# Kernel tuning notes

Hardware: AMD Instinct MI355X
Metric: run time of the kernel (lower is better)

The kernel has to match this reference:

```python
import jax, jax.numpy as jnp
import numpy as np

B = 4
C = 128           # input channels
H = W = 512       # image size
P = 16            # patch size
GH = GW = 32      # token grid (H//P, W//P)
N = GH * GW       # num patches = 1024
PATCH_DIM = C * P * P  # 32768
DIM = 512         # embed dim
MLP = 256         # ffn hidden
DH = 64           # dim per head
HEADS = (2, 4, 8) # per-layer head counts
NUM_REL = (2 * GH - 1) * (2 * GW - 1)  # 3969


def _rel_index():
    # faithful to the torch buffer construction (meshgrid default 'ij')
    coords = np.stack(np.meshgrid(np.arange(GH), np.arange(GW), indexing='ij')).reshape(2, -1)
    rc = (coords[:, :, None] - coords[:, None, :]).transpose(1, 2, 0)  # [N,N,2]
    rc[..., 0] += GH - 1
    rc[..., 1] += GW - 1
    rc[..., 0] *= 2 * GH - 1
    return jnp.asarray(rc.sum(-1))  # [N,N] int

REL_IDX = _rel_index()


def _ln(x, s, b):
    m = x.mean(-1, keepdims=True)
    v = x.var(-1, keepdims=True)
    return (x - m) / jnp.sqrt(v + 1e-5) * s + b


def setup_inputs() -> dict:
    key = jax.random.key(0)
    ks = iter(jax.random.split(key, 40))
    def rn(shape, scale=0.02):
        return jax.random.normal(next(ks), shape, jnp.float32) * scale
    inp = {"img": jax.random.normal(next(ks), (B, C, H, W), jnp.float32)}
    inp["patch_w"] = rn((PATCH_DIM, DIM))
    inp["patch_b"] = jnp.zeros((DIM,), jnp.float32)
    inp["pos_emb"] = rn((1, N, DIM), 1.0)
    inp["ln1_s"] = jnp.ones((3, DIM), jnp.float32)
    inp["ln1_b"] = jnp.zeros((3, DIM), jnp.float32)
    inp["ln2_s"] = jnp.ones((3, DIM), jnp.float32)
    inp["ln2_b"] = jnp.zeros((3, DIM), jnp.float32)
    for l, h in enumerate(HEADS):
        inner = DH * h
        inp[f"qkv_w{l}"] = rn((DIM, 3 * inner))
        inp[f"out_w{l}"] = rn((inner, DIM))
        inp[f"out_b{l}"] = jnp.zeros((DIM,), jnp.float32)
        inp[f"bias{l}"] = rn((NUM_REL, h))
    inp["ff_w1"] = rn((3, DIM, MLP))
    inp["ff_b1"] = jnp.zeros((3, MLP), jnp.float32)
    inp["ff_w2"] = rn((3, MLP, DIM))
    inp["ff_b2"] = jnp.zeros((3, DIM), jnp.float32)
    return inp


def reference(img, patch_w, patch_b, pos_emb, ln1_s, ln1_b, ln2_s, ln2_b,
              qkv_w0, qkv_w1, qkv_w2, out_w0, out_w1, out_w2,
              out_b0, out_b1, out_b2, bias0, bias1, bias2,
              ff_w1, ff_b1, ff_w2, ff_b2):
    b = img.shape[0]
    # Rearrange 'b c (h p1) (w p2) -> b (h w) (p1 p2 c)'
    x = img.reshape(b, C, GH, P, GW, P).transpose(0, 2, 4, 3, 5, 1).reshape(b, N, PATCH_DIM)
    x = x @ patch_w + patch_b + pos_emb

    qkv_ws = (qkv_w0, qkv_w1, qkv_w2)
    out_ws = (out_w0, out_w1, out_w2)
    out_bs = (out_b0, out_b1, out_b2)
    tables = (bias0, bias1, bias2)

    for l, h in enumerate(HEADS):
        # attention with relative position bias
        xn = _ln(x, ln1_s[l], ln1_b[l])
        qkv = xn @ qkv_ws[l]                                  # [b, N, 3*h*DH]
        q, k, v = jnp.split(qkv, 3, axis=-1)
        q = q.reshape(b, N, h, DH).transpose(0, 2, 1, 3)      # bhnd
        k = k.reshape(b, N, h, DH).transpose(0, 2, 1, 3)
        v = v.reshape(b, N, h, DH).transpose(0, 2, 1, 3)
        dots = jnp.einsum('bhnd,bhmd->bhnm', q, k) * (DH ** -0.5)
        rel = tables[l][REL_IDX].transpose(2, 0, 1)           # [h, N, N]
        attn = jax.nn.softmax(dots + rel[None], axis=-1)
        o = jnp.einsum('bhnm,bhmd->bhnd', attn, v)
        o = o.transpose(0, 2, 1, 3).reshape(b, N, h * DH)
        x = o @ out_ws[l] + out_bs[l] + x
        # feed-forward
        xn = _ln(x, ln2_s[l], ln2_b[l])
        hmid = jax.nn.gelu(xn @ ff_w1[l] + ff_b1[l], approximate=False)
        x = hmid @ ff_w2[l] + ff_b2[l] + x

    return x.transpose(0, 2, 1).reshape(b, DIM, GH, GW)
```

## Files before the change

### kernel.cpp

```cpp
#include <hip/hip_runtime.h>

typedef unsigned short u16;
typedef __bf16 bf16x8 __attribute__((ext_vector_type(8)));
typedef float f32x4 __attribute__((ext_vector_type(4)));

#define AS1 __attribute__((address_space(1)))
#define AS3 __attribute__((address_space(3)))
#define MFMA(a,b,c) __builtin_amdgcn_mfma_f32_16x16x32_bf16(a,b,c,0,0,0)

__device__ __forceinline__ u16 f2bf(float f) {
    union { float f; unsigned u; } x; x.f = f;
    unsigned r = x.u + 0x7fffu + ((x.u >> 16) & 1u);
    return (u16)(r >> 16);
}

__global__ void k_patch_wT(const float* __restrict__ w, u16* __restrict__ o)
{
    __shared__ u16 T[256*33];
    int c = blockIdx.x, n0 = blockIdx.y*32;
    int t = threadIdx.x;
    int rr = t >> 5, cc = t & 31;
    #pragma unroll
    for (int i = 0; i < 32; ++i) {
        int r = i*8 + rr;
        int k = (r >> 4)*2048 + (r & 15)*128 + c;
        T[r*33 + cc] = f2bf(w[(size_t)k*512 + n0 + cc]);
    }
    __syncthreads();
    #pragma unroll
    for (int i = 0; i < 4; ++i) {
        int j  = i*8 + (t >> 5);
        int ch = t & 31;
        union { u16 u[8]; uint4 v; } pk;
        #pragma unroll
        for (int q = 0; q < 8; ++q) pk.u[q] = T[(ch*8+q)*33 + j];
        *(uint4*)(o + (size_t)(n0 + j)*32768 + c*256 + ch*8) = pk.v;
    }
}

struct TXJob { const float* in; u16* out; int K, N, tiles; };
struct TXArgs { TXJob j[12]; };

__global__ void k_wT_all(TXArgs a)
{
    __shared__ float T[32*33];
    int bid = blockIdx.x;
    int ji = 0;
    while (bid >= a.j[ji].tiles) { bid -= a.j[ji].tiles; ++ji; }
    const float* __restrict__ in = a.j[ji].in;
    u16* __restrict__ o = a.j[ji].out;
    const int K = a.j[ji].K, N = a.j[ji].N;
    const int tn = N >> 5;
    const int kt = (bid / tn) * 32, nt = (bid % tn) * 32;
    int t = threadIdx.x, r = t >> 5, c = t & 31;
    #pragma unroll
    for (int i = 0; i < 4; ++i)
        T[(r + i*8)*33 + c] = in[(size_t)(kt + r + i*8)*N + nt + c];
    __syncthreads();
    #pragma unroll
    for (int i = 0; i < 4; ++i)
        o[(size_t)(nt + r + i*8)*K + kt + c] = f2bf(T[c*33 + r + i*8]);
}

__global__ __launch_bounds__(1024) void k_patch_gemm(
    const float* __restrict__ img, const u16* __restrict__ Bt, float* __restrict__ part)
{
    __shared__ alignas(16) u16 As[2*128*64];
    __shared__ alignas(16) u16 Bs[2*512*64];
    const int t = threadIdx.x;
    const int bid = blockIdx.x;
    const int z = bid & 7;
    const int tile = bid >> 3;
    const int b = tile >> 3, gh0 = (tile & 7)*4;
    const int m0 = tile*128;
    const int wave = t >> 6, lane = t & 63;
    const int r16 = lane & 15, g = lane >> 4;
    const int wm = (wave >> 3)*64, wn = (wave & 7)*64;

    const int arow = t >> 6;
    const int ghl = arow >> 2, p1l = arow & 3;
    const int aw = (t & 63)*8;
    const int tok = ghl*32 + (aw >> 4);
    unsigned abyte = (unsigned)(tok*128 + p1l*32 + (aw & 15)*2);
    abyte ^= (unsigned)((tok & 7) << 4);
    const float* imgb = img + (size_t)b*128*262144
                      + (size_t)((gh0 + ghl)*16 + p1l)*512 + aw;
    const int brow = t >> 3;
    const int bchunk = (t & 7) ^ (brow & 7);
    const u16* Bb = Bt + (size_t)brow*32768 + (size_t)z*4096 + bchunk*8;
    u16* Bsd = Bs + t*8;

    f32x4 acc[4][4];
    const f32x4 zz = {0.f,0.f,0.f,0.f};
    #pragma unroll
    for (int im = 0; im < 4; ++im)
        #pragma unroll
        for (int in_ = 0; in_ < 4; ++in_) acc[im][in_] = zz;

#define STAGE(KC, BUF) do {                                                          \
    const int c_ = z*16 + ((KC) >> 2);                                               \
    const float* src_ = imgb + (size_t)c_*262144 + ((KC) & 3)*2048;                  \
    float4 a0_ = *(const float4*)src_;                                               \
    float4 a1_ = *(const float4*)(src_ + 4);                                         \
    _Pragma("unroll")                                                                \
    for (int i_ = 0; i_ < 4; ++i_)                                                   \
        __builtin_amdgcn_global_load_lds((AS1 void*)(Bb + (size_t)i_*128*32768 + (KC)*64), \
                                         (AS3 void*)(Bsd + (BUF)*32768 + i_*8192), 16, 0, 0); \
    union { u16 u[8]; uint4 v; } pk_;                                                \
    pk_.u[0]=f2bf(a0_.x); pk_.u[1]=f2bf(a0_.y); pk_.u[2]=f2bf(a0_.z); pk_.u[3]=f2bf(a0_.w); \
    pk_.u[4]=f2bf(a1_.x); pk_.u[5]=f2bf(a1_.y); pk_.u[6]=f2bf(a1_.z); pk_.u[7]=f2bf(a1_.w); \
    *(uint4*)((char*)As + (BUF)*16384 + abyte) = pk_.v;                              \
} while(0)

    STAGE(0, 0);
    __syncthreads();
    int cur = 0;
    for (int kc = 0; kc < 64; ++kc) {
        if (kc < 63) STAGE(kc + 1, cur ^ 1);
        const char* Asb = (const char*)As + cur*16384;
        const char* Bsb = (const char*)Bs + cur*65536;
        #pragma unroll
        for (int kk = 0; kk < 64; kk += 32) {
            bf16x8 af[4], bfr[4];
            #pragma unroll
            for (int im = 0; im < 4; ++im) {
                unsigned off = ((unsigned)((wm + im*16 + r16)*128 + kk*2 + g*16))
                             ^ (unsigned)((r16 & 7) << 4);
                af[im] = *(const bf16x8*)(Asb + off);
            }
            #pragma unroll
            for (int in_ = 0; in_ < 4; ++in_) {
                unsigned off = ((unsigned)((wn + in_*16 + r16)*128 + kk*2 + g*16))
                             ^ (unsigned)((r16 & 7) << 4);
                bfr[in_] = *(const bf16x8*)(Bsb + off);
            }
            #pragma unroll
            for (int im = 0; im < 4; ++im)
                #pragma unroll
                for (int in_ = 0; in_ < 4; ++in_)
                    acc[im][in_] = MFMA(af[im], bfr[in_], acc[im][in_]);
        }
        __syncthreads();
        cur ^= 1;
    }
#undef STAGE
    float* pz = part + (size_t)z*4096*512;
    #pragma unroll
    for (int im = 0; im < 4; ++im) {
        int row = m0 + wm + im*16 + g*4;
        #pragma unroll
        for (int in_ = 0; in_ < 4; ++in_) {
            int col = wn + in_*16 + r16;
            #pragma unroll
            for (int r = 0; r < 4; ++r)
                pz[(size_t)(row + r)*512 + col] = acc[im][in_][r];
        }
    }
}

__global__ void k_reduce_ln(const float* __restrict__ part,
                            const float* __restrict__ pb, const float* __restrict__ pe,
                            const float* __restrict__ sc, const float* __restrict__ bi,
                            float* __restrict__ x, u16* __restrict__ xn)
{
    int row = blockIdx.x, lane = threadIdx.x;
    int d = lane*8;
    size_t rbase = (size_t)row*512 + d;
    float4 a0 = *(const float4*)(pb + d);
    float4 a1 = *(const float4*)(pb + d + 4);
    size_t pebase = (size_t)(row & 1023)*512 + d;
    float4 p0 = *(const float4*)(pe + pebase);
    float4 p1 = *(const float4*)(pe + pebase + 4);
    float vv[8] = {a0.x+p0.x, a0.y+p0.y, a0.z+p0.z, a0.w+p0.w,
                   a1.x+p1.x, a1.y+p1.y, a1.z+p1.z, a1.w+p1.w};
    #pragma unroll
    for (int z = 0; z < 8; ++z) {
        const float* pr = part + (size_t)z*4096*512 + rbase;
        float4 q0 = *(const float4*)pr;
        float4 q1 = *(const float4*)(pr + 4);
        vv[0] += q0.x; vv[1] += q0.y; vv[2] += q0.z; vv[3] += q0.w;
        vv[4] += q1.x; vv[5] += q1.y; vv[6] += q1.z; vv[7] += q1.w;
    }
    float4 w0 = make_float4(vv[0], vv[1], vv[2], vv[3]);
    float4 w1 = make_float4(vv[4], vv[5], vv[6], vv[7]);
    *(float4*)(x + rbase) = w0;
    *(float4*)(x + rbase + 4) = w1;
    float sum = 0.f, sq = 0.f;
    #pragma unroll
    for (int i = 0; i < 8; ++i) { sum += vv[i]; sq += vv[i]*vv[i]; }
    #pragma unroll
    for (int m = 1; m < 64; m <<= 1) { sum += __shfl_xor(sum, m, 64); sq += __shfl_xor(sq, m, 64); }
    float mean = sum * (1.f/512.f);
    float var  = sq  * (1.f/512.f) - mean*mean;
    float rstd = rsqrtf(var + 1e-5f);
    union { u16 u[8]; uint4 v; } pk;
    #pragma unroll
    for (int i = 0; i < 8; ++i) pk.u[i] = f2bf((vv[i]-mean)*rstd*sc[d+i] + bi[d+i]);
    *(uint4*)(xn + rbase) = pk.v;
}

__global__ void k_ln(const float* __restrict__ x, const float* __restrict__ sc,
                     const float* __restrict__ bi, u16* __restrict__ o)
{
    int row = blockIdx.x, lane = threadIdx.x;
    const float* xr = x + (size_t)row*512 + lane*8;
    float4 v0 = *(const float4*)xr;
    float4 v1 = *(const float4*)(xr + 4);
    float vv[8] = {v0.x,v0.y,v0.z,v0.w,v1.x,v1.y,v1.z,v1.w};
    float sum = 0.f, sq = 0.f;
    #pragma unroll
    for (int i = 0; i < 8; ++i) { sum += vv[i]; sq += vv[i]*vv[i]; }
    #pragma unroll
    for (int m = 1; m < 64; m <<= 1) { sum += __shfl_xor(sum, m, 64); sq += __shfl_xor(sq, m, 64); }
    float mean = sum * (1.f/512.f);
    float var  = sq  * (1.f/512.f) - mean*mean;
    float rstd = rsqrtf(var + 1e-5f);
    int d = lane*8;
    union { u16 u[8]; uint4 v; } pk;
    #pragma unroll
    for (int i = 0; i < 8; ++i) pk.u[i] = f2bf((vv[i]-mean)*rstd*sc[d+i] + bi[d+i]);
    *(uint4*)(o + (size_t)row*512 + d) = pk.v;
}

template<int EPI, int KB>
__global__ __launch_bounds__(256) void k_gemm(
    const u16* __restrict__ A, int lda,
    const u16* __restrict__ Bt, int ldb,
    float* __restrict__ Cf, u16* __restrict__ Cb, int ldc,
    const float* __restrict__ bias)
{
    __shared__ alignas(16) u16 As[128*64];
    __shared__ alignas(16) u16 Bs[128*64];
    const int t = threadIdx.x;
    const int m0 = blockIdx.x*128, n0 = blockIdx.y*128;
    const int wave = t >> 6, lane = t & 63;
    const int wm = (wave >> 1)*64, wn = (wave & 1)*64;
    const int r16 = lane & 15, g = lane >> 4;
    const u16* Ab = A + (size_t)(m0 + (t>>3))*lda + (t&7)*8;
    const u16* Bb = Bt + (size_t)(n0 + (t>>3))*ldb + (t&7)*8;
    u16* Asd = As + t*8;
    u16* Bsd = Bs + t*8;
    f32x4 acc[4][4];
    const f32x4 z4 = {0.f,0.f,0.f,0.f};
    #pragma unroll
    for (int im = 0; im < 4; ++im)
        #pragma unroll
        for (int in_ = 0; in_ < 4; ++in_) acc[im][in_] = z4;

    #pragma unroll
    for (int k = 0; k < KB; k += 64) {
        #pragma unroll
        for (int i = 0; i < 4; ++i) {
            __builtin_amdgcn_global_load_lds((AS1 void*)(Ab + (size_t)i*32*lda + k), (AS3 void*)(Asd + i*2048), 16, 0, 0);
            __builtin_amdgcn_global_load_lds((AS1 void*)(Bb + (size_t)i*32*ldb + k), (AS3 void*)(Bsd + i*2048), 16, 0, 0);
        }
        __syncthreads();
        #pragma unroll
        for (int kk = 0; kk < 64; kk += 32) {
            bf16x8 af[4], bfr[4];
            #pragma unroll
            for (int im = 0; im < 4; ++im)
                af[im] = *(const bf16x8*)(As + (wm + im*16 + r16)*64 + kk + g*8);
            #pragma unroll
            for (int in_ = 0; in_ < 4; ++in_)
                bfr[in_] = *(const bf16x8*)(Bs + (wn + in_*16 + r16)*64 + kk + g*8);
            #pragma unroll
            for (int im = 0; im < 4; ++im)
                #pragma unroll
                for (int in_ = 0; in_ < 4; ++in_)
                    acc[im][in_] = MFMA(af[im], bfr[in_], acc[im][in_]);
        }
        __syncthreads();
    }
    #pragma unroll
    for (int im = 0; im < 4; ++im) {
        int row = m0 + wm + im*16 + g*4;
        #pragma unroll
        for (int in_ = 0; in_ < 4; ++in_) {
            int col = n0 + wn + in_*16 + r16;
            #pragma unroll
            for (int r = 0; r < 4; ++r) {
                float v = acc[im][in_][r];
                size_t idx = (size_t)(row + r)*ldc + col;
                if constexpr (EPI == 1) {
                    Cb[idx] = f2bf(v);
                } else if constexpr (EPI == 2) {
                    float xv = v + bias[col];
                    Cb[idx] = f2bf(0.5f*xv*(1.f + erff(xv*0.70710678118654752f)));
                } else {
                    Cf[idx] += v + bias[col];
                }
            }
        }
    }
}

__global__ __launch_bounds__(256) void k_attn(
    const u16* __restrict__ qkv, const float* __restrict__ bt,
    u16* __restrict__ o, int H)
{
    const int LD = 80;
    __shared__ alignas(16) u16 Qs[64*80], Ks[64*80], Vs[64*80];
    __shared__ alignas(16) u16 Ps[4][16*80];
    const int inner = H*64, s3 = 3*inner;
    const int qt = blockIdx.x, head = blockIdx.y, b = blockIdx.z;
    const int t = threadIdx.x, wave = t >> 6, lane = t & 63;
    const int r16 = lane & 15, g = lane >> 4;
    const int q0 = qt*64;
    const size_t tokbase = (size_t)b*1024;
    const int hoff = head*64;

    #pragma unroll
    for (int it = 0; it < 2; ++it) {
        int flat = it*256 + t, r = flat >> 3, d0 = (flat & 7)*8;
        uint4 v = *(const uint4*)(qkv + (tokbase + q0 + r)*s3 + hoff + d0);
        *(uint4*)(Qs + r*LD + d0) = v;
    }
    __syncthreads();
    bf16x8 aQ0 = *(const bf16x8*)(Qs + (wave*16 + r16)*LD + g*8);
    bf16x8 aQ1 = *(const bf16x8*)(Qs + (wave*16 + r16)*LD + 32 + g*8);

    float m_[4], l_[4];
    f32x4 O[4];
    const f32x4 z4 = {0.f,0.f,0.f,0.f};
    #pragma unroll
    for (int r = 0; r < 4; ++r) { m_[r] = -1e30f; l_[r] = 0.f; O[r] = z4; }
    const int qg_base = q0 + wave*16 + g*4;

    for (int kt = 0; kt < 16; ++kt) {
        const int key0 = kt*64;
        #pragma unroll
        for (int it = 0; it < 2; ++it) {
            int flat = it*256 + t, r = flat >> 3, d0 = (flat & 7)*8;
            uint4 v = *(const uint4*)(qkv + (tokbase + key0 + r)*s3 + inner + hoff + d0);
            *(uint4*)(Ks + r*LD + d0) = v;
        }
        #pragma unroll
        for (int it = 0; it < 2; ++it) {
            int flat = it*256 + t, key = flat & 63, d0 = (flat >> 6)*8;
            uint4 v = *(const uint4*)(qkv + (tokbase + key0 + key)*s3 + 2*inner + hoff + d0);
            const u16* pv = (const u16*)&v;
            #pragma unroll
            for (int i = 0; i < 8; ++i) Vs[(d0+i)*LD + key] = pv[i];
        }
        __syncthreads();

        float Sv[4][4];
        #pragma unroll
        for (int kb = 0; kb < 4; ++kb) {
            bf16x8 k0f = *(const bf16x8*)(Ks + (kb*16 + r16)*LD + g*8);
            bf16x8 k1f = *(const bf16x8*)(Ks + (kb*16 + r16)*LD + 32 + g*8);
            f32x4 S = z4;
            S = MFMA(aQ0, k0f, S);
            S = MFMA(aQ1, k1f, S);
            int keyg = key0 + kb*16 + r16;
            int kgh = keyg >> 5, kgw = keyg & 31;
            #pragma unroll
            for (int r = 0; r < 4; ++r) {
                int qg = qg_base + r;
                int rel = ((qg >> 5) - kgh + 31)*63 + ((qg & 31) - kgw + 31);
                Sv[kb][r] = S[r]*0.125f + bt[rel*H + head];
            }
        }
        float mx[4], al[4], ps[4];
        #pragma unroll
        for (int r = 0; r < 4; ++r)
            mx[r] = fmaxf(fmaxf(Sv[0][r], Sv[1][r]), fmaxf(Sv[2][r], Sv[3][r]));
        #pragma unroll
        for (int msk = 1; msk < 16; msk <<= 1)
            #pragma unroll
            for (int r = 0; r < 4; ++r) mx[r] = fmaxf(mx[r], __shfl_xor(mx[r], msk, 64));
        #pragma unroll
        for (int r = 0; r < 4; ++r) {
            float nm = fmaxf(m_[r], mx[r]);
            al[r] = __expf(m_[r] - nm);
            m_[r] = nm;
            ps[r] = 0.f;
        }
        #pragma unroll
        for (int kb = 0; kb < 4; ++kb)
            #pragma unroll
            for (int r = 0; r < 4; ++r) {
                float p = __expf(Sv[kb][r] - m_[r]);
                Sv[kb][r] = p;
                ps[r] += p;
            }
        #pragma unroll
        for (int msk = 1; msk < 16; msk <<= 1)
            #pragma unroll
            for (int r = 0; r < 4; ++r) ps[r] += __shfl_xor(ps[r], msk, 64);
        #pragma unroll
        for (int r = 0; r < 4; ++r) l_[r] = l_[r]*al[r] + ps[r];
        #pragma unroll
        for (int kb = 0; kb < 4; ++kb)
            #pragma unroll
            for (int r = 0; r < 4; ++r)
                Ps[wave][(g*4 + r)*LD + kb*16 + r16] = f2bf(Sv[kb][r]);
        #pragma unroll
        for (int dt = 0; dt < 4; ++dt)
            #pragma unroll
            for (int r = 0; r < 4; ++r) O[dt][r] = O[dt][r]*al[r];
        __syncthreads();
        bf16x8 aP0 = *(const bf16x8*)(Ps[wave] + r16*LD + g*8);
        bf16x8 aP1 = *(const bf16x8*)(Ps[wave] + r16*LD + 32 + g*8);
        #pragma unroll
        for (int dt = 0; dt < 4; ++dt) {
            bf16x8 v0 = *(const bf16x8*)(Vs + (dt*16 + r16)*LD + g*8);
            bf16x8 v1 = *(const bf16x8*)(Vs + (dt*16 + r16)*LD + 32 + g*8);
            O[dt] = MFMA(aP0, v0, O[dt]);
            O[dt] = MFMA(aP1, v1, O[dt]);
        }
        __syncthreads();
    }
    #pragma unroll
    for (int dt = 0; dt < 4; ++dt)
        #pragma unroll
        for (int r = 0; r < 4; ++r) {
            int token = q0 + wave*16 + g*4 + r;
            o[(tokbase + token)*inner + hoff + dt*16 + r16] = f2bf(O[dt][r] / l_[r]);
        }
}

__global__ void k_out_transpose(const float* __restrict__ x, float* __restrict__ o)
{
    __shared__ float T[32*33];
    int d0 = blockIdx.x*32, n0 = blockIdx.y*32, b = blockIdx.z;
    int t = threadIdx.x, r = t >> 5, c = t & 31;
    #pragma unroll
    for (int i = 0; i < 4; ++i)
        T[(r+i*8)*33 + c] = x[((size_t)b*1024 + n0 + r + i*8)*512 + d0 + c];
    __syncthreads();
    #pragma unroll
    for (int i = 0; i < 4; ++i)
        o[((size_t)b*512 + d0 + r + i*8)*1024 + n0 + c] = T[c*33 + (r+i*8)];
}

extern "C" void kernel_launch(void* const* d_in, const int* in_sizes, int n_in,
                              void* d_out, int out_size, void* d_ws, size_t ws_size,
                              hipStream_t stream)
{
    (void)in_sizes; (void)n_in; (void)out_size; (void)ws_size;
    const float* img     = (const float*)d_in[0];
    const float* patch_w = (const float*)d_in[1];
    const float* patch_b = (const float*)d_in[2];
    const float* pos_emb = (const float*)d_in[3];
    const float* ln1_s   = (const float*)d_in[4];
    const float* ln1_b   = (const float*)d_in[5];
    const float* ln2_s   = (const float*)d_in[6];
    const float* ln2_b   = (const float*)d_in[7];
    const float* qkv_w[3] = {(const float*)d_in[8],  (const float*)d_in[12], (const float*)d_in[16]};
    const float* out_w[3] = {(const float*)d_in[9],  (const float*)d_in[13], (const float*)d_in[17]};
    const float* out_b[3] = {(const float*)d_in[10], (const float*)d_in[14], (const float*)d_in[18]};
    const float* biasT[3] = {(const float*)d_in[11], (const float*)d_in[15], (const float*)d_in[19]};
    const float* ff_w1 = (const float*)d_in[20];
    const float* ff_b1 = (const float*)d_in[21];
    const float* ff_w2 = (const float*)d_in[22];
    const float* ff_b2 = (const float*)d_in[23];
    float* out = (float*)d_out;

    const int HS[3] = {2, 4, 8};

    char* ws = (char*)d_ws;
    size_t off = 0;
    auto alloc = [&](size_t bytes) -> void* {
        void* p = ws + off; off += (bytes + 255) & ~(size_t)255; return p;
    };
    u16*   pwT  = (u16*)  alloc(512ull*32768*2);
    float* x    = (float*)alloc(4096ull*512*4);
    u16*   xn   = (u16*)  alloc(4096ull*512*2);
    u16*   qkv  = (u16*)  alloc(4096ull*1536*2);
    u16*   ob   = (u16*)  alloc(4096ull*512*2);
    u16*   mid  = (u16*)  alloc(4096ull*256*2);
    u16*   qkvT = (u16*)  alloc(2688ull*512*2);
    u16*   outT = (u16*)  alloc(512ull*896*2);
    u16*   f1T  = (u16*)  alloc(3ull*256*512*2);
    u16*   f2T  = (u16*)  alloc(3ull*512*256*2);
    float* part = (float*)alloc(8ull*4096*512*4);

    u16* qkvT_l[3] = { qkvT, qkvT + 384ull*512, qkvT + (384ull+768)*512 };
    u16* outT_l[3] = { outT, outT + 512ull*128, outT + 512ull*(128+256) };
    u16* f1T_l[3]  = { f1T,  f1T  + 256ull*512, f1T  + 2ull*256*512 };
    u16* f2T_l[3]  = { f2T,  f2T  + 512ull*256, f2T  + 2ull*512*256 };

    k_patch_wT<<<dim3(128,16), 256, 0, stream>>>(patch_w, pwT);

    TXArgs tx;
    int tj = 0, total_tiles = 0;
    auto add_job = [&](const float* in, u16* o, int K, int N) {
        tx.j[tj] = TXJob{in, o, K, N, (K/32)*(N/32)};
        total_tiles += tx.j[tj].tiles; ++tj;
    };
    for (int l = 0; l < 3; ++l) add_job(qkv_w[l], qkvT_l[l], 512, 3*64*HS[l]);
    for (int l = 0; l < 3; ++l) add_job(out_w[l], outT_l[l], 64*HS[l], 512);
    for (int l = 0; l < 3; ++l) add_job(ff_w1 + (size_t)l*512*256, f1T_l[l], 512, 256);
    for (int l = 0; l < 3; ++l) add_job(ff_w2 + (size_t)l*256*512, f2T_l[l], 256, 512);
    k_wT_all<<<total_tiles, 256, 0, stream>>>(tx);

    k_patch_gemm<<<256, 1024, 0, stream>>>(img, pwT, part);
    k_reduce_ln<<<4096, 64, 0, stream>>>(part, patch_b, pos_emb,
                                         ln1_s, ln1_b, x, xn);

    for (int l = 0; l < 3; ++l) {
        int h = HS[l], inner = 64*h, n3 = 3*inner;

        if (l > 0)
            k_ln<<<4096, 64, 0, stream>>>(x, ln1_s + l*512, ln1_b + l*512, xn);
        k_gemm<1,512><<<dim3(32, n3/128), 256, 0, stream>>>(xn, 512, qkvT_l[l], 512,
                                                            nullptr, qkv, n3, nullptr);
        k_attn<<<dim3(16, h, 4), 256, 0, stream>>>(qkv, biasT[l], ob, h);
        if (l == 0)
            k_gemm<3,128><<<dim3(32, 4), 256, 0, stream>>>(ob, inner, outT_l[l], inner,
                                                           x, nullptr, 512, out_b[l]);
        else if (l == 1)
            k_gemm<3,256><<<dim3(32, 4), 256, 0, stream>>>(ob, inner, outT_l[l], inner,
                                                           x, nullptr, 512, out_b[l]);
        else
            k_gemm<3,512><<<dim3(32, 4), 256, 0, stream>>>(ob, inner, outT_l[l], inner,
                                                           x, nullptr, 512, out_b[l]);
        k_ln<<<4096, 64, 0, stream>>>(x, ln2_s + l*512, ln2_b + l*512, xn);
        k_gemm<2,512><<<dim3(32, 2), 256, 0, stream>>>(xn, 512, f1T_l[l], 512,
                                                       nullptr, mid, 256, ff_b1 + l*256);
        k_gemm<3,256><<<dim3(32, 4), 256, 0, stream>>>(mid, 256, f2T_l[l], 256,
                                                       x, nullptr, 512, ff_b2 + l*512);
    }
    k_out_transpose<<<dim3(16, 32, 4), 256, 0, stream>>>(x, out);
}
```

Measured before the change: 722.1 us.

## Shrink patch GEMM and layer GEMM M-tiles to raise block count

The patch-embedding GEMM moves from 1024-thread blocks with 128-row tiles and a K-chunk of 64 to 512-thread blocks with 64-row tiles and a K-chunk of 32. This doubles the grid to 512 blocks and rewrites the image staging, the LDS swizzle and the B-load addressing to match. The generic k_gemm gains a BM template parameter, and all layer GEMMs now use 64-row tiles with twice as many blocks. The aim is better CU occupancy and load balance on the small-M GEMMs, at the cost of less reuse per block, more global traffic for the B operand and more barriers.

Measured after the change: 736.5 us. Within noise of the previous version (+2.0%).

```diff
diff --git a/kernel.cpp b/kernel.cpp
--- a/kernel.cpp
+++ b/kernel.cpp
@@ -62,32 +62,30 @@
         o[(size_t)(nt + r + i*8)*K + kt + c] = f2bf(T[c*33 + r + i*8]);
 }
 
-__global__ __launch_bounds__(1024) void k_patch_gemm(
+__global__ __launch_bounds__(512) void k_patch_gemm(
     const float* __restrict__ img, const u16* __restrict__ Bt, float* __restrict__ part)
 {
-    __shared__ alignas(16) u16 As[2*128*64];
-    __shared__ alignas(16) u16 Bs[2*512*64];
+    __shared__ alignas(16) u16 As[2*64*32];
+    __shared__ alignas(16) u16 Bs[2*512*32];
     const int t = threadIdx.x;
     const int bid = blockIdx.x;
     const int z = bid & 7;
     const int tile = bid >> 3;
-    const int b = tile >> 3, gh0 = (tile & 7)*4;
-    const int m0 = tile*128;
+    const int b = tile >> 4, gh0 = (tile & 15)*2;
+    const int m0 = tile*64;
     const int wave = t >> 6, lane = t & 63;
     const int r16 = lane & 15, g = lane >> 4;
-    const int wm = (wave >> 3)*64, wn = (wave & 7)*64;
-
-    const int arow = t >> 6;
-    const int ghl = arow >> 2, p1l = arow & 3;
-    const int aw = (t & 63)*8;
-    const int tok = ghl*32 + (aw >> 4);
-    unsigned abyte = (unsigned)(tok*128 + p1l*32 + (aw & 15)*2);
-    abyte ^= (unsigned)((tok & 7) << 4);
-    const float* imgb = img + (size_t)b*128*262144
-                      + (size_t)((gh0 + ghl)*16 + p1l)*512 + aw;
-    const int brow = t >> 3;
-    const int bchunk = (t & 7) ^ (brow & 7);
-    const u16* Bb = Bt + (size_t)brow*32768 + (size_t)z*4096 + bchunk*8;
+    const int wn = wave*64;
+
+    const int r4 = t >> 7;
+    const int ghl = r4 >> 1, p1o = r4 & 1;
+    const int c4 = (t & 127)*4;
+    const int tok = ghl*32 + (c4 >> 4);
+    const int p2 = c4 & 15;
+    const unsigned abyte = (unsigned)(tok*64 + ((p1o*32 + p2*2) ^ (((tok >> 1) & 3) << 4)));
+    const float* imgb = img + ((size_t)(b*128 + z*16)*512 + (gh0 + ghl)*16 + p1o)*512 + c4;
+    const u16* Bb = Bt + (size_t)(t >> 2)*32768 + (size_t)z*4096
+                  + (((t & 3)*8) ^ (((t >> 3) & 3) << 3));
     u16* Bsd = Bs + t*8;
 
     f32x4 acc[4][4];
@@ -98,48 +96,37 @@
         for (int in_ = 0; in_ < 4; ++in_) acc[im][in_] = zz;
 
 #define STAGE(KC, BUF) do {                                                          \
-    const int c_ = z*16 + ((KC) >> 2);                                               \
-    const float* src_ = imgb + (size_t)c_*262144 + ((KC) & 3)*2048;                  \
-    float4 a0_ = *(const float4*)src_;                                               \
-    float4 a1_ = *(const float4*)(src_ + 4);                                         \
+    const float* s_ = imgb + (size_t)((KC) >> 3)*262144 + ((KC) & 7)*1024;           \
+    float4 a0_ = *(const float4*)s_;                                                 \
     _Pragma("unroll")                                                                \
     for (int i_ = 0; i_ < 4; ++i_)                                                   \
-        __builtin_amdgcn_global_load_lds((AS1 void*)(Bb + (size_t)i_*128*32768 + (KC)*64), \
-                                         (AS3 void*)(Bsd + (BUF)*32768 + i_*8192), 16, 0, 0); \
-    union { u16 u[8]; uint4 v; } pk_;                                                \
+        __builtin_amdgcn_global_load_lds((AS1 void*)(Bb + (size_t)i_*128*32768 + (KC)*32), \
+                                         (AS3 void*)(Bsd + (BUF)*16384 + i_*4096), 16, 0, 0); \
+    union { u16 u[4]; unsigned long long v; } pk_;                                   \
     pk_.u[0]=f2bf(a0_.x); pk_.u[1]=f2bf(a0_.y); pk_.u[2]=f2bf(a0_.z); pk_.u[3]=f2bf(a0_.w); \
-    pk_.u[4]=f2bf(a1_.x); pk_.u[5]=f2bf(a1_.y); pk_.u[6]=f2bf(a1_.z); pk_.u[7]=f2bf(a1_.w); \
-    *(uint4*)((char*)As + (BUF)*16384 + abyte) = pk_.v;                              \
+    *(unsigned long long*)((char*)As + (BUF)*4096 + abyte) = pk_.v;                  \
 } while(0)
 
+    const unsigned sw = ((unsigned)((r16 >> 1) & 3)) << 4;
     STAGE(0, 0);
     __syncthreads();
     int cur = 0;
-    for (int kc = 0; kc < 64; ++kc) {
-        if (kc < 63) STAGE(kc + 1, cur ^ 1);
-        const char* Asb = (const char*)As + cur*16384;
-        const char* Bsb = (const char*)Bs + cur*65536;
-        #pragma unroll
-        for (int kk = 0; kk < 64; kk += 32) {
-            bf16x8 af[4], bfr[4];
-            #pragma unroll
-            for (int im = 0; im < 4; ++im) {
-                unsigned off = ((unsigned)((wm + im*16 + r16)*128 + kk*2 + g*16))
-                             ^ (unsigned)((r16 & 7) << 4);
-                af[im] = *(const bf16x8*)(Asb + off);
-            }
-            #pragma unroll
-            for (int in_ = 0; in_ < 4; ++in_) {
-                unsigned off = ((unsigned)((wn + in_*16 + r16)*128 + kk*2 + g*16))
-                             ^ (unsigned)((r16 & 7) << 4);
-                bfr[in_] = *(const bf16x8*)(Bsb + off);
-            }
-            #pragma unroll
-            for (int im = 0; im < 4; ++im)
-                #pragma unroll
-                for (int in_ = 0; in_ < 4; ++in_)
-                    acc[im][in_] = MFMA(af[im], bfr[in_], acc[im][in_]);
-        }
+    for (int kc = 0; kc < 128; ++kc) {
+        if (kc < 127) STAGE(kc + 1, cur ^ 1);
+        const char* Asb = (const char*)As + cur*4096;
+        const char* Bsb = (const char*)Bs + cur*32768;
+        bf16x8 af[4], bfr[4];
+        #pragma unroll
+        for (int im = 0; im < 4; ++im)
+            af[im] = *(const bf16x8*)(Asb + (im*16 + r16)*64 + ((unsigned)(g*16) ^ sw));
+        #pragma unroll
+        for (int in_ = 0; in_ < 4; ++in_)
+            bfr[in_] = *(const bf16x8*)(Bsb + (wn + in_*16 + r16)*64 + ((unsigned)(g*16) ^ sw));
+        #pragma unroll
+        for (int im = 0; im < 4; ++im)
+            #pragma unroll
+            for (int in_ = 0; in_ < 4; ++in_)
+                acc[im][in_] = MFMA(af[im], bfr[in_], acc[im][in_]);
         __syncthreads();
         cur ^= 1;
     }
@@ -147,7 +134,7 @@
     float* pz = part + (size_t)z*4096*512;
     #pragma unroll
     for (int im = 0; im < 4; ++im) {
-        int row = m0 + wm + im*16 + g*4;
+        int row = m0 + im*16 + g*4;
         #pragma unroll
         for (int in_ = 0; in_ < 4; ++in_) {
             int col = wn + in_*16 + r16;
@@ -222,50 +209,52 @@
     *(uint4*)(o + (size_t)row*512 + d) = pk.v;
 }
 
-template<int EPI, int KB>
+template<int EPI, int KB, int BM>
 __global__ __launch_bounds__(256) void k_gemm(
     const u16* __restrict__ A, int lda,
     const u16* __restrict__ Bt, int ldb,
     float* __restrict__ Cf, u16* __restrict__ Cb, int ldc,
     const float* __restrict__ bias)
 {
-    __shared__ alignas(16) u16 As[128*64];
+    constexpr int MI = BM/32;
+    __shared__ alignas(16) u16 As[BM*64];
     __shared__ alignas(16) u16 Bs[128*64];
     const int t = threadIdx.x;
-    const int m0 = blockIdx.x*128, n0 = blockIdx.y*128;
+    const int m0 = blockIdx.x*BM, n0 = blockIdx.y*128;
     const int wave = t >> 6, lane = t & 63;
-    const int wm = (wave >> 1)*64, wn = (wave & 1)*64;
+    const int wm = (wave >> 1)*(16*MI), wn = (wave & 1)*64;
     const int r16 = lane & 15, g = lane >> 4;
     const u16* Ab = A + (size_t)(m0 + (t>>3))*lda + (t&7)*8;
     const u16* Bb = Bt + (size_t)(n0 + (t>>3))*ldb + (t&7)*8;
     u16* Asd = As + t*8;
     u16* Bsd = Bs + t*8;
-    f32x4 acc[4][4];
+    f32x4 acc[MI][4];
     const f32x4 z4 = {0.f,0.f,0.f,0.f};
     #pragma unroll
-    for (int im = 0; im < 4; ++im)
+    for (int im = 0; im < MI; ++im)
         #pragma unroll
         for (int in_ = 0; in_ < 4; ++in_) acc[im][in_] = z4;
 
     #pragma unroll
     for (int k = 0; k < KB; k += 64) {
         #pragma unroll
-        for (int i = 0; i < 4; ++i) {
+        for (int i = 0; i < BM/32; ++i)
             __builtin_amdgcn_global_load_lds((AS1 void*)(Ab + (size_t)i*32*lda + k), (AS3 void*)(Asd + i*2048), 16, 0, 0);
+        #pragma unroll
+        for (int i = 0; i < 4; ++i)
             __builtin_amdgcn_global_load_lds((AS1 void*)(Bb + (size_t)i*32*ldb + k), (AS3 void*)(Bsd + i*2048), 16, 0, 0);
-        }
         __syncthreads();
         #pragma unroll
         for (int kk = 0; kk < 64; kk += 32) {
-            bf16x8 af[4], bfr[4];
-            #pragma unroll
-            for (int im = 0; im < 4; ++im)
+            bf16x8 af[MI], bfr[4];
+            #pragma unroll
+            for (int im = 0; im < MI; ++im)
                 af[im] = *(const bf16x8*)(As + (wm + im*16 + r16)*64 + kk + g*8);
             #pragma unroll
             for (int in_ = 0; in_ < 4; ++in_)
                 bfr[in_] = *(const bf16x8*)(Bs + (wn + in_*16 + r16)*64 + kk + g*8);
             #pragma unroll
-            for (int im = 0; im < 4; ++im)
+            for (int im = 0; im < MI; ++im)
                 #pragma unroll
                 for (int in_ = 0; in_ < 4; ++in_)
                     acc[im][in_] = MFMA(af[im], bfr[in_], acc[im][in_]);
@@ -273,7 +262,7 @@
         __syncthreads();
     }
     #pragma unroll
-    for (int im = 0; im < 4; ++im) {
+    for (int im = 0; im < MI; ++im) {
         int row = m0 + wm + im*16 + g*4;
         #pragma unroll
         for (int in_ = 0; in_ < 4; ++in_) {
@@ -496,7 +485,7 @@
     for (int l = 0; l < 3; ++l) add_job(ff_w2 + (size_t)l*256*512, f2T_l[l], 256, 512);
     k_wT_all<<<total_tiles, 256, 0, stream>>>(tx);
 
-    k_patch_gemm<<<256, 1024, 0, stream>>>(img, pwT, part);
+    k_patch_gemm<<<512, 512, 0, stream>>>(img, pwT, part);
     k_reduce_ln<<<4096, 64, 0, stream>>>(part, patch_b, pos_emb,
                                          ln1_s, ln1_b, x, xn);
 
@@ -505,23 +494,23 @@
 
         if (l > 0)
             k_ln<<<4096, 64, 0, stream>>>(x, ln1_s + l*512, ln1_b + l*512, xn);
-        k_gemm<1,512><<<dim3(32, n3/128), 256, 0, stream>>>(xn, 512, qkvT_l[l], 512,
-                                                            nullptr, qkv, n3, nullptr);
+        k_gemm<1,512,64><<<dim3(64, n3/128), 256, 0, stream>>>(xn, 512, qkvT_l[l], 512,
+                                                               nullptr, qkv, n3, nullptr);
         k_attn<<<dim3(16, h, 4), 256, 0, stream>>>(qkv, biasT[l], ob, h);
         if (l == 0)
-            k_gemm<3,128><<<dim3(32, 4), 256, 0, stream>>>(ob, inner, outT_l[l], inner,
-                                                           x, nullptr, 512, out_b[l]);
+            k_gemm<3,128,64><<<dim3(64, 4), 256, 0, stream>>>(ob, inner, outT_l[l], inner,
+                                                              x, nullptr, 512, out_b[l]);
         else if (l == 1)
-            k_gemm<3,256><<<dim3(32, 4), 256, 0, stream>>>(ob, inner, outT_l[l], inner,
-                                                           x, nullptr, 512, out_b[l]);
+            k_gemm<3,256,64><<<dim3(64, 4), 256, 0, stream>>>(ob, inner, outT_l[l], inner,
+                                                              x, nullptr, 512, out_b[l]);
         else
-            k_gemm<3,512><<<dim3(32, 4), 256, 0, stream>>>(ob, inner, outT_l[l], inner,
-                                                           x, nullptr, 512, out_b[l]);
+            k_gemm<3,512,64><<<dim3(64, 4), 256, 0, stream>>>(ob, inner, outT_l[l], inner,
+                                                              x, nullptr, 512, out_b[l]);
         k_ln<<<4096, 64, 0, stream>>>(x, ln2_s + l*512, ln2_b + l*512, xn);
-        k_gemm<2,512><<<dim3(32, 2), 256, 0, stream>>>(xn, 512, f1T_l[l], 512,
-                                                       nullptr, mid, 256, ff_b1 + l*256);
-        k_gemm<3,256><<<dim3(32, 4), 256, 0, stream>>>(mid, 256, f2T_l[l], 256,
-                                                       x, nullptr, 512, ff_b2 + l*512);
+        k_gemm<2,512,64><<<dim3(64, 2), 256, 0, stream>>>(xn, 512, f1T_l[l], 512,
+                                                          nullptr, mid, 256, ff_b1 + l*256);
+        k_gemm<3,256,64><<<dim3(64, 4), 256, 0, stream>>>(mid, 256, f2T_l[l], 256,
+                                                          x, nullptr, 512, ff_b2 + l*512);
     }
     k_out_transpose<<<dim3(16, 32, 4), 256, 0, stream>>>(x, out);
 }
```
